# Performance work log

Measured on AMD Instinct MI355X. Metric: run time of the kernel, lower is better.

## Reference

```python
import jax, jax.numpy as jnp
import numpy as np

N, C_IN, C_K, C_V, H = 8192, 512, 512, 512, 8


def setup_inputs() -> dict:
    key = jax.random.key(0)
    ks = jax.random.split(key, 9)
    s = 0.02
    return {
        "input_": jax.random.normal(ks[0], (N, C_IN), dtype=jnp.float32),
        "Wk": jax.random.normal(ks[1], (C_IN, C_K), dtype=jnp.float32) * s,
        "bk": jnp.zeros((C_K,), dtype=jnp.float32),
        "Wq": jax.random.normal(ks[2], (C_IN, C_K), dtype=jnp.float32) * s,
        "bq": jnp.zeros((C_K,), dtype=jnp.float32),
        "Wv": jax.random.normal(ks[3], (C_IN, C_V), dtype=jnp.float32) * s,
        "bv": jnp.zeros((C_V,), dtype=jnp.float32),
        "Wr": jax.random.normal(ks[4], (C_K, C_K), dtype=jnp.float32) * s,
        "br": jnp.zeros((C_K,), dtype=jnp.float32),
    }


def reference(input_, Wk, bk, Wq, bq, Wv, bv, Wr, br):
    n = input_.shape[0]
    keys = input_ @ Wk + bk      # [N, C_K]
    queries = input_ @ Wq + bq   # [N, C_K]
    values = input_ @ Wv + bv    # [N, C_V]
    hk = C_K // H
    hv = C_V // H
    # [H, N, hk] / [H, N, hv]
    k = keys.reshape(n, H, hk).transpose(1, 0, 2)
    q = queries.reshape(n, H, hk).transpose(1, 0, 2)
    v = values.reshape(n, H, hv).transpose(1, 0, 2)
    k_sm = jax.nn.softmax(k, axis=1)   # softmax over tokens (dim=0 in torch)
    q_sm = jax.nn.softmax(q, axis=2)   # softmax over head channels (dim=1)
    # context = key^T @ value per head: [H, hk, hv]
    context = jnp.einsum('hnk,hnv->hkv', k_sm, v)
    attended = jnp.einsum('hnk,hkv->hnv', q_sm, context)  # [H, N, hv]
    # concat heads along channel dim -> [N, C_V]
    aggregated = attended.transpose(1, 0, 2).reshape(n, C_V)
    attention = aggregated @ Wr + br
    # mean over heads of q_sm @ k_sm^T; contracting h and k jointly = one GEMM
    scores = jnp.einsum('hnk,hmk->nm', q_sm, k_sm) / H  # [N, N]
    return attention, scores
```

## Files before the change

### kernel.cpp

```cpp
#include <hip/hip_runtime.h>

#define NT 8192
#define CD 512
#define NH 8
#define SC_N 8192

using f32x4  = __attribute__((ext_vector_type(4))) float;
using bf16x8 = __attribute__((ext_vector_type(8))) __bf16;

__device__ __forceinline__ unsigned short f2bf(float x) {
    union { float f; unsigned u; } c; c.f = x;
    unsigned r = c.u + 0x7fffu + ((c.u >> 16) & 1u);
    return (unsigned short)(r >> 16);
}
__device__ __forceinline__ float bf2f(unsigned short b) {
    union { float f; unsigned u; } c; c.u = ((unsigned)b) << 16;
    return c.f;
}

__global__ void prep_k(const float4* __restrict__ in, unsigned short* __restrict__ out,
                       const float* __restrict__ Wk, const float* __restrict__ Wq,
                       const float* __restrict__ Wv, const float* __restrict__ bk,
                       const float* __restrict__ bq, const float* __restrict__ bv,
                       unsigned short* __restrict__ Wt, float* __restrict__ biaskqv) {
    int b = blockIdx.x;
    if (b < 4096) {
        int i = b * 256 + threadIdx.x;
        float4 v = in[i];
        out[i*4+0] = f2bf(v.x);
        out[i*4+1] = f2bf(v.y);
        out[i*4+2] = f2bf(v.z);
        out[i*4+3] = f2bf(v.w);
    } else {
        int idx = (b - 4096) * 256 + threadIdx.x;
        int c = idx >> 9, k = idx & 511;
        int sec = c >> 9, cc = c & 511;
        const float* W = (sec == 0) ? Wk : ((sec == 1) ? Wq : Wv);
        Wt[idx] = f2bf(W[k * 512 + cc]);
        if (idx < 1536) {
            const float* bb = (idx < 512) ? bk : ((idx < 1024) ? bq : bv);
            biaskqv[idx] = bb[idx & 511];
        }
    }
}

__global__ __launch_bounds__(256) void kqv_gemm_k(
    const unsigned short* __restrict__ A, const unsigned short* __restrict__ Bt,
    const float* __restrict__ bias,
    unsigned short* __restrict__ kbf, unsigned short* __restrict__ qsm,
    unsigned short* __restrict__ vbf,
    float* __restrict__ pmax, float* __restrict__ psum)
{
    __shared__ unsigned short sA[128 * 32];
    __shared__ unsigned short sB[128 * 32];
    const int tid  = threadIdx.x;
    const int wid  = tid >> 6;
    const int lane = tid & 63;
    const int col0 = blockIdx.x * 128;
    const int row0 = blockIdx.y * 128;
    const int by   = blockIdx.y;
    const int wr = (wid >> 1) * 64;
    const int wc = (wid & 1) * 64;
    const int fr = lane & 15;
    const int fq = lane >> 4;
    const int srow = lane >> 2;
    const int scol = (lane & 3) * 8;

    f32x4 acc[4][4] = {};

    for (int kt = 0; kt < 16; ++kt) {
        const int k0 = kt << 5;
        __syncthreads();
        #pragma unroll
        for (int s = 0; s < 2; ++s) {
            const int seg = wid * 2 + s;
            const unsigned short* gA = A + (size_t)(row0 + seg * 16 + srow) * 512 + k0 + scol;
            __builtin_amdgcn_global_load_lds(
                (const __attribute__((address_space(1))) void*)gA,
                (__attribute__((address_space(3))) void*)(sA + seg * 512), 16, 0, 0);
            const unsigned short* gB = Bt + (size_t)(col0 + seg * 16 + srow) * 512 + k0 + scol;
            __builtin_amdgcn_global_load_lds(
                (const __attribute__((address_space(1))) void*)gB,
                (__attribute__((address_space(3))) void*)(sB + seg * 512), 16, 0, 0);
        }
        __syncthreads();

        bf16x8 av[4], bfrag[4];
        #pragma unroll
        for (int m = 0; m < 4; ++m)
            av[m] = *(const bf16x8*)(sA + (wr + m * 16 + fr) * 32 + fq * 8);
        #pragma unroll
        for (int n = 0; n < 4; ++n)
            bfrag[n] = *(const bf16x8*)(sB + (wc + n * 16 + fr) * 32 + fq * 8);
        #pragma unroll
        for (int m = 0; m < 4; ++m)
            #pragma unroll
            for (int n = 0; n < 4; ++n)
                acc[m][n] = __builtin_amdgcn_mfma_f32_16x16x32_bf16(av[m], bfrag[n], acc[m][n], 0, 0, 0);
    }

    const int sec = col0 >> 9;
    const int cs0 = (col0 & 511) + wc;

    if (sec == 0) {
        const int pb = by * 2 + (wr >> 6);
        #pragma unroll
        for (int n = 0; n < 4; ++n) {
            const int col = cs0 + n * 16 + fr;
            const float bv = bias[col];
            float vv[4][4], mx = -1e30f;
            #pragma unroll
            for (int m = 0; m < 4; ++m)
                #pragma unroll
                for (int r = 0; r < 4; ++r) {
                    float x = bf2f(f2bf(acc[m][n][r] + bv));
                    vv[m][r] = x; mx = fmaxf(mx, x);
                }
            mx = fmaxf(mx, __shfl_xor(mx, 16));
            mx = fmaxf(mx, __shfl_xor(mx, 32));
            float s = 0.f;
            #pragma unroll
            for (int m = 0; m < 4; ++m)
                #pragma unroll
                for (int r = 0; r < 4; ++r) {
                    s += __expf(vv[m][r] - mx);
                    kbf[(size_t)(row0 + wr + m * 16 + fq * 4 + r) * 512 + col] = f2bf(vv[m][r]);
                }
            s += __shfl_xor(s, 16);
            s += __shfl_xor(s, 32);
            if (lane < 16) { pmax[pb * 512 + col] = mx; psum[pb * 512 + col] = s; }
        }
    } else if (sec == 1) {
        #pragma unroll
        for (int m = 0; m < 4; ++m)
            #pragma unroll
            for (int r = 0; r < 4; ++r) {
                float e[4], mx = -1e30f;
                #pragma unroll
                for (int n = 0; n < 4; ++n) {
                    float x = bf2f(f2bf(acc[m][n][r] + bias[512 + cs0 + n * 16 + fr]));
                    e[n] = x; mx = fmaxf(mx, x);
                }
                mx = fmaxf(mx, __shfl_xor(mx, 1));
                mx = fmaxf(mx, __shfl_xor(mx, 2));
                mx = fmaxf(mx, __shfl_xor(mx, 4));
                mx = fmaxf(mx, __shfl_xor(mx, 8));
                float s = 0.f;
                #pragma unroll
                for (int n = 0; n < 4; ++n) { e[n] = __expf(e[n] - mx); s += e[n]; }
                s += __shfl_xor(s, 1);
                s += __shfl_xor(s, 2);
                s += __shfl_xor(s, 4);
                s += __shfl_xor(s, 8);
                const float rs = 1.f / s;
                const int row = row0 + wr + m * 16 + fq * 4 + r;
                #pragma unroll
                for (int n = 0; n < 4; ++n)
                    qsm[(size_t)row * 512 + cs0 + n * 16 + fr] = f2bf(e[n] * rs);
            }
    } else {
        #pragma unroll
        for (int n = 0; n < 4; ++n) {
            const int col = cs0 + n * 16 + fr;
            const float bv = bias[1024 + col];
            #pragma unroll
            for (int m = 0; m < 4; ++m)
                #pragma unroll
                for (int r = 0; r < 4; ++r)
                    vbf[(size_t)(row0 + wr + m * 16 + fq * 4 + r) * 512 + col] = f2bf(acc[m][n][r] + bv);
        }
    }
}

__global__ __launch_bounds__(256) void ksmctx_k(
    const unsigned short* __restrict__ kbf, const unsigned short* __restrict__ vbf,
    const float* __restrict__ pmax, const float* __restrict__ psum,
    unsigned short* __restrict__ ksm, float* __restrict__ pctx)
{
    const int ch = blockIdx.x;
    const int h  = blockIdx.y;
    const int tid = threadIdx.x, w = tid >> 6, lane = tid & 63;
    const int fr = lane & 15, fq = lane >> 4;
    __shared__ unsigned short tr[4][2][4096];
    __shared__ float redm[4][64], reds[4][64], cmx[64], crc[64];

    {
        const int c = tid & 63, q = tid >> 6;
        const int col = h * 64 + c;
        float m = -1e30f;
        for (int r = 0; r < 32; ++r) m = fmaxf(m, pmax[(q * 32 + r) * 512 + col]);
        float s = 0.f;
        for (int r = 0; r < 32; ++r)
            s += psum[(q * 32 + r) * 512 + col] * __expf(pmax[(q * 32 + r) * 512 + col] - m);
        redm[q][c] = m; reds[q][c] = s;
    }
    __syncthreads();
    if (tid < 64) {
        float m = fmaxf(fmaxf(redm[0][tid], redm[1][tid]), fmaxf(redm[2][tid], redm[3][tid]));
        float s = 0.f;
        #pragma unroll
        for (int q = 0; q < 4; ++q) s += reds[q][tid] * __expf(redm[q][tid] - m);
        cmx[tid] = m; crc[tid] = 1.f / s;
    }
    __syncthreads();

    char* kt = (char*)&tr[w][0][0];
    char* vt = (char*)&tr[w][1][0];
    const int nbase = ch * 256 + w * 64;
    #pragma unroll
    for (int j = 0; j < 8; ++j) {
        bf16x8 kv = *(const bf16x8*)(kbf + (size_t)(nbase + lane) * 512 + h * 64 + j * 8);
        bf16x8 vv = *(const bf16x8*)(vbf + (size_t)(nbase + lane) * 512 + h * 64 + j * 8);
        unsigned short ko[8];
        #pragma unroll
        for (int e = 0; e < 8; ++e) {
            int k = j * 8 + e;
            float x = __expf(bf2f(((const unsigned short*)&kv)[e]) - cmx[k]) * crc[k];
            unsigned short us = f2bf(x);
            ko[e] = us;
            int byte = (k * 128 + lane * 2) ^ (e << 4);
            *(unsigned short*)(kt + byte) = us;
            *(unsigned short*)(vt + byte) = ((const unsigned short*)&vv)[e];
        }
        *(uint4*)(ksm + (size_t)(nbase + lane) * 512 + h * 64 + j * 8) = *(const uint4*)ko;
    }
    asm volatile("s_waitcnt lgkmcnt(0)" ::: "memory");
    __builtin_amdgcn_sched_barrier(0);

    f32x4 acc[4][4] = {};
    #pragma unroll
    for (int ks = 0; ks < 2; ++ks) {
        bf16x8 a[4], b[4];
        #pragma unroll
        for (int mf = 0; mf < 4; ++mf) {
            int row  = mf * 16 + fr;
            int byte = (row * 128 + (ks * 4 + fq) * 16) ^ ((row & 7) << 4);
            a[mf] = *(const bf16x8*)(kt + byte);
            b[mf] = *(const bf16x8*)(vt + byte);
        }
        #pragma unroll
        for (int mf = 0; mf < 4; ++mf)
            #pragma unroll
            for (int nf = 0; nf < 4; ++nf)
                acc[mf][nf] = __builtin_amdgcn_mfma_f32_16x16x32_bf16(a[mf], b[nf], acc[mf][nf], 0, 0, 0);
    }

    float* red = (float*)&tr[w][0][0];
    #pragma unroll
    for (int mf = 0; mf < 4; ++mf)
        #pragma unroll
        for (int nf = 0; nf < 4; ++nf)
            #pragma unroll
            for (int r = 0; r < 4; ++r) {
                int lr = mf * 16 + fq * 4 + r;
                int lc = (nf * 16 + fr) ^ (((lr >> 2) & 1) << 4);
                red[lr * 64 + lc] = acc[mf][nf][r];
            }
    __syncthreads();
    const float* rbase = (const float*)&tr[0][0][0];
    float* out = pctx + (size_t)(ch * 8 + h) * 4096;
    #pragma unroll
    for (int it = 0; it < 16; ++it) {
        int e = it * 256 + tid;
        int lr = e >> 6;
        int ph = (lr * 64) + ((e & 63) ^ (((lr >> 2) & 1) << 4));
        float s = rbase[ph] + rbase[4096 + ph] + rbase[8192 + ph] + rbase[12288 + ph];
        out[e] = s;
    }
}

__global__ void mtred_k(const float* __restrict__ pctx, const float* __restrict__ Wr,
                        unsigned short* __restrict__ Mt) {
    __shared__ float cr[64];
    const int b = blockIdx.x;
    const int hk = b >> 1;
    const int o  = (b & 1) * 256 + threadIdx.x;
    const int h = hk >> 6, k = hk & 63;
    if (threadIdx.x < 64) {
        float s = 0.f;
        for (int p = 0; p < 32; ++p)
            s += pctx[(size_t)(p * 8 + h) * 4096 + k * 64 + threadIdx.x];
        cr[threadIdx.x] = s;
    }
    __syncthreads();
    const float* wp = Wr + (size_t)(h * 64) * 512 + o;
    float s = 0.f;
    #pragma unroll
    for (int j = 0; j < 64; ++j)
        s += cr[j] * wp[(size_t)j * 512];
    Mt[(size_t)o * 512 + hk] = f2bf(s);
}

__global__ __launch_bounds__(256) void scores_attn_k(
    const unsigned short* __restrict__ qsm, const unsigned short* __restrict__ ksm,
    const unsigned short* __restrict__ Mt, const float* __restrict__ br,
    float* __restrict__ attn_out, float* __restrict__ scores_out)
{
    __shared__ unsigned short sA[128 * 32];
    __shared__ unsigned short sB[128 * 32];
    const int tid  = threadIdx.x;
    const int wid  = tid >> 6;
    const int lane = tid & 63;
    const int wr = (wid >> 1) * 64;
    const int wc = (wid & 1) * 64;
    const int fr = lane & 15;
    const int fq = lane >> 4;
    const int srow = lane >> 2;
    const int scol = (lane & 3) * 8;

    const bool is_attn = blockIdx.x < 256;
    int row0, col0;
    const unsigned short* Bt;
    if (is_attn) {
        const int bx = blockIdx.x;
        col0 = (bx & 3) * 128;
        row0 = (bx >> 2) * 128;
        Bt = Mt;
    } else {
        int g = blockIdx.x - 256;
        g = (g & 7) * 512 + (g >> 3);
        row0 = ((g & 7) + ((g >> 9) << 3)) * 128;
        col0 = ((g >> 3) & 63) * 128;
        Bt = ksm;
    }

    f32x4 acc[4][4] = {};

    for (int kt = 0; kt < 16; ++kt) {
        const int k0 = kt << 5;
        __syncthreads();
        #pragma unroll
        for (int s = 0; s < 2; ++s) {
            const int seg = wid * 2 + s;
            const unsigned short* gA = qsm + (size_t)(row0 + seg * 16 + srow) * 512 + k0 + scol;
            __builtin_amdgcn_global_load_lds(
                (const __attribute__((address_space(1))) void*)gA,
                (__attribute__((address_space(3))) void*)(sA + seg * 512), 16, 0, 0);
            const unsigned short* gB = Bt + (size_t)(col0 + seg * 16 + srow) * 512 + k0 + scol;
            __builtin_amdgcn_global_load_lds(
                (const __attribute__((address_space(1))) void*)gB,
                (__attribute__((address_space(3))) void*)(sB + seg * 512), 16, 0, 0);
        }
        __syncthreads();

        bf16x8 av[4], bfrag[4];
        #pragma unroll
        for (int m = 0; m < 4; ++m)
            av[m] = *(const bf16x8*)(sA + (wr + m * 16 + fr) * 32 + fq * 8);
        #pragma unroll
        for (int n = 0; n < 4; ++n)
            bfrag[n] = *(const bf16x8*)(sB + (wc + n * 16 + fr) * 32 + fq * 8);
        #pragma unroll
        for (int m = 0; m < 4; ++m)
            #pragma unroll
            for (int n = 0; n < 4; ++n)
                acc[m][n] = __builtin_amdgcn_mfma_f32_16x16x32_bf16(av[m], bfrag[n], acc[m][n], 0, 0, 0);
    }

    if (is_attn) {
        #pragma unroll
        for (int n = 0; n < 4; ++n) {
            const int col = col0 + wc + n * 16 + fr;
            const float bval = br[col];
            #pragma unroll
            for (int m = 0; m < 4; ++m) {
                #pragma unroll
                for (int r = 0; r < 4; ++r) {
                    const int row = row0 + wr + m * 16 + fq * 4 + r;
                    __builtin_nontemporal_store(acc[m][n][r] + bval, &attn_out[(size_t)row * 512 + col]);
                }
            }
        }
    } else {
        #pragma unroll
        for (int n = 0; n < 4; ++n) {
            const int col = col0 + wc + n * 16 + fr;
            #pragma unroll
            for (int m = 0; m < 4; ++m) {
                #pragma unroll
                for (int r = 0; r < 4; ++r) {
                    const int row = row0 + wr + m * 16 + fq * 4 + r;
                    __builtin_nontemporal_store(acc[m][n][r] * 0.125f, &scores_out[(size_t)row * SC_N + col]);
                }
            }
        }
    }
}

extern "C" void kernel_launch(void* const* d_in, const int* in_sizes, int n_in,
                              void* d_out, int out_size, void* d_ws, size_t ws_size,
                              hipStream_t stream) {
    const float* input = (const float*)d_in[0];
    const float* Wk = (const float*)d_in[1];
    const float* bk = (const float*)d_in[2];
    const float* Wq = (const float*)d_in[3];
    const float* bq = (const float*)d_in[4];
    const float* Wv = (const float*)d_in[5];
    const float* bv = (const float*)d_in[6];
    const float* Wr = (const float*)d_in[7];
    const float* br = (const float*)d_in[8];

    char* ws = (char*)d_ws;
    unsigned short* inp_bf = (unsigned short*)ws;  ws += (size_t)NT * CD * 2;
    unsigned short* Wt     = (unsigned short*)ws;  ws += (size_t)1536 * 512 * 2;
    float* biaskqv         = (float*)ws;           ws += 1536 * 4;
    unsigned short* kbf    = (unsigned short*)ws;  ws += (size_t)NT * CD * 2;
    unsigned short* qsm    = (unsigned short*)ws;  ws += (size_t)NT * CD * 2;
    unsigned short* vbf    = (unsigned short*)ws;  ws += (size_t)NT * CD * 2;
    unsigned short* ksm    = (unsigned short*)ws;  ws += (size_t)NT * CD * 2;
    float* pmax            = (float*)ws;           ws += 128 * 512 * 4;
    float* psum            = (float*)ws;           ws += 128 * 512 * 4;
    float* pctx            = (float*)ws;           ws += (size_t)32 * 8 * 4096 * 4;
    unsigned short* Mt     = (unsigned short*)ws;  ws += (size_t)512 * 512 * 2;

    float* attn_out   = (float*)d_out;
    float* scores_out = (float*)d_out + (size_t)NT * CD;

    prep_k<<<7168, 256, 0, stream>>>((const float4*)input, inp_bf,
                                     Wk, Wq, Wv, bk, bq, bv, Wt, biaskqv);

    kqv_gemm_k<<<dim3(12, 64), 256, 0, stream>>>(inp_bf, Wt, biaskqv,
                                                 kbf, qsm, vbf, pmax, psum);

    ksmctx_k<<<dim3(32, 8), 256, 0, stream>>>(kbf, vbf, pmax, psum, ksm, pctx);

    mtred_k<<<1024, 256, 0, stream>>>(pctx, Wr, Mt);

    scores_attn_k<<<4352, 256, 0, stream>>>(qsm, ksm, Mt, br, attn_out, scores_out);
}
```

Baseline: 177.3 us.

## Double K-tile depth to 64 and XOR-swizzle LDS layout in scores GEMM

```diff
diff --git a/kernel.cpp b/kernel.cpp
--- a/kernel.cpp
+++ b/kernel.cpp
@@ -296,8 +296,8 @@
     const unsigned short* __restrict__ Mt, const float* __restrict__ br,
     float* __restrict__ attn_out, float* __restrict__ scores_out)
 {
-    __shared__ unsigned short sA[128 * 32];
-    __shared__ unsigned short sB[128 * 32];
+    __shared__ unsigned short sA[128 * 64];
+    __shared__ unsigned short sB[128 * 64];
     const int tid  = threadIdx.x;
     const int wid  = tid >> 6;
     const int lane = tid & 63;
@@ -305,8 +305,6 @@
     const int wc = (wid & 1) * 64;
     const int fr = lane & 15;
     const int fq = lane >> 4;
-    const int srow = lane >> 2;
-    const int scol = (lane & 3) * 8;
 
     const bool is_attn = blockIdx.x < 256;
     int row0, col0;
@@ -324,37 +322,58 @@
         Bt = ksm;
     }
 
+    int srow[4], sk8[4];
+    #pragma unroll
+    for (int l = 0; l < 4; ++l) {
+        int i = l * 256 + tid;
+        srow[l] = i >> 3;
+        sk8[l]  = ((i & 7) ^ ((i >> 3) & 7)) * 8;
+    }
+
+    int offA[4][2], offB[4][2];
+    #pragma unroll
+    for (int m = 0; m < 4; ++m)
+        #pragma unroll
+        for (int ks = 0; ks < 2; ++ks) {
+            int ra = wr + m * 16 + fr;
+            offA[m][ks] = ra * 128 + (((ks * 4 + fq) ^ (ra & 7)) << 4);
+            int rb = wc + m * 16 + fr;
+            offB[m][ks] = rb * 128 + (((ks * 4 + fq) ^ (rb & 7)) << 4);
+        }
+
     f32x4 acc[4][4] = {};
 
-    for (int kt = 0; kt < 16; ++kt) {
-        const int k0 = kt << 5;
+    for (int kt = 0; kt < 8; ++kt) {
+        const int k0 = kt << 6;
         __syncthreads();
         #pragma unroll
-        for (int s = 0; s < 2; ++s) {
-            const int seg = wid * 2 + s;
-            const unsigned short* gA = qsm + (size_t)(row0 + seg * 16 + srow) * 512 + k0 + scol;
+        for (int l = 0; l < 4; ++l) {
+            const unsigned short* gA = qsm + (size_t)(row0 + srow[l]) * 512 + k0 + sk8[l];
             __builtin_amdgcn_global_load_lds(
                 (const __attribute__((address_space(1))) void*)gA,
-                (__attribute__((address_space(3))) void*)(sA + seg * 512), 16, 0, 0);
-            const unsigned short* gB = Bt + (size_t)(col0 + seg * 16 + srow) * 512 + k0 + scol;
+                (__attribute__((address_space(3))) void*)(sA + (l * 256 + wid * 64) * 8), 16, 0, 0);
+            const unsigned short* gB = Bt + (size_t)(col0 + srow[l]) * 512 + k0 + sk8[l];
             __builtin_amdgcn_global_load_lds(
                 (const __attribute__((address_space(1))) void*)gB,
-                (__attribute__((address_space(3))) void*)(sB + seg * 512), 16, 0, 0);
+                (__attribute__((address_space(3))) void*)(sB + (l * 256 + wid * 64) * 8), 16, 0, 0);
         }
         __syncthreads();
 
-        bf16x8 av[4], bfrag[4];
+        bf16x8 av[4][2], bv[4][2];
         #pragma unroll
         for (int m = 0; m < 4; ++m)
-            av[m] = *(const bf16x8*)(sA + (wr + m * 16 + fr) * 32 + fq * 8);
-        #pragma unroll
-        for (int n = 0; n < 4; ++n)
-            bfrag[n] = *(const bf16x8*)(sB + (wc + n * 16 + fr) * 32 + fq * 8);
-        #pragma unroll
-        for (int m = 0; m < 4; ++m)
-            #pragma unroll
-            for (int n = 0; n < 4; ++n)
-                acc[m][n] = __builtin_amdgcn_mfma_f32_16x16x32_bf16(av[m], bfrag[n], acc[m][n], 0, 0, 0);
+            #pragma unroll
+            for (int ks = 0; ks < 2; ++ks) {
+                av[m][ks] = *(const bf16x8*)((const char*)sA + offA[m][ks]);
+                bv[m][ks] = *(const bf16x8*)((const char*)sB + offB[m][ks]);
+            }
+        #pragma unroll
+        for (int ks = 0; ks < 2; ++ks)
+            #pragma unroll
+            for (int m = 0; m < 4; ++m)
+                #pragma unroll
+                for (int n = 0; n < 4; ++n)
+                    acc[m][n] = __builtin_amdgcn_mfma_f32_16x16x32_bf16(av[m][ks], bv[n][ks], acc[m][n], 0, 0, 0);
     }
 
     if (is_attn) {
```

Result: slower. 183.8 us (+3.7%).

## Fuse Mt reduction into ksmctx via atomic counter and enlarge scores tile

Applied to the files above, without the earlier changes.

```diff
diff --git a/kernel.cpp b/kernel.cpp
--- a/kernel.cpp
+++ b/kernel.cpp
@@ -22,8 +22,10 @@
                        const float* __restrict__ Wk, const float* __restrict__ Wq,
                        const float* __restrict__ Wv, const float* __restrict__ bk,
                        const float* __restrict__ bq, const float* __restrict__ bv,
-                       unsigned short* __restrict__ Wt, float* __restrict__ biaskqv) {
+                       unsigned short* __restrict__ Wt, float* __restrict__ biaskqv,
+                       int* __restrict__ cnt) {
     int b = blockIdx.x;
+    if (b == 0 && threadIdx.x == 0) *cnt = 0;
     if (b < 4096) {
         int i = b * 256 + threadIdx.x;
         float4 v = in[i];
@@ -175,7 +177,9 @@
 __global__ __launch_bounds__(256) void ksmctx_k(
     const unsigned short* __restrict__ kbf, const unsigned short* __restrict__ vbf,
     const float* __restrict__ pmax, const float* __restrict__ psum,
-    unsigned short* __restrict__ ksm, float* __restrict__ pctx)
+    unsigned short* __restrict__ ksm, float* __restrict__ pctx,
+    const float* __restrict__ Wr, unsigned short* __restrict__ Mt,
+    int* __restrict__ cnt)
 {
     const int ch = blockIdx.x;
     const int h  = blockIdx.y;
@@ -183,6 +187,7 @@
     const int fr = lane & 15, fq = lane >> 4;
     __shared__ unsigned short tr[4][2][4096];
     __shared__ float redm[4][64], reds[4][64], cmx[64], crc[64];
+    __shared__ int lold;
 
     {
         const int c = tid & 63, q = tid >> 6;
@@ -267,28 +272,41 @@
         float s = rbase[ph] + rbase[4096 + ph] + rbase[8192 + ph] + rbase[12288 + ph];
         out[e] = s;
     }
-}
-
-__global__ void mtred_k(const float* __restrict__ pctx, const float* __restrict__ Wr,
-                        unsigned short* __restrict__ Mt) {
-    __shared__ float cr[64];
-    const int b = blockIdx.x;
-    const int hk = b >> 1;
-    const int o  = (b & 1) * 256 + threadIdx.x;
-    const int h = hk >> 6, k = hk & 63;
-    if (threadIdx.x < 64) {
-        float s = 0.f;
-        for (int p = 0; p < 32; ++p)
-            s += pctx[(size_t)(p * 8 + h) * 4096 + k * 64 + threadIdx.x];
-        cr[threadIdx.x] = s;
-    }
+
+    __threadfence();
     __syncthreads();
-    const float* wp = Wr + (size_t)(h * 64) * 512 + o;
-    float s = 0.f;
-    #pragma unroll
-    for (int j = 0; j < 64; ++j)
-        s += cr[j] * wp[(size_t)j * 512];
-    Mt[(size_t)o * 512 + hk] = f2bf(s);
+    if (tid == 0) lold = atomicAdd(cnt, 1);
+    __syncthreads();
+    const int old = lold;
+    if (old >= 224) {
+        if (tid == 0) { while (atomicAdd(cnt, 0) < 256) __builtin_amdgcn_s_sleep(2); }
+        __syncthreads();
+        __threadfence();
+        const int ti = old - 224;
+        float* cr = (float*)&tr[0][0][0];
+        for (int u = 0; u < 16; ++u) {
+            const int hk = ti * 16 + u;
+            const int hh = hk >> 6, kk = hk & 63;
+            if (tid < 64) {
+                float s = 0.f;
+                for (int p = 0; p < 32; ++p)
+                    s += pctx[(size_t)(p * 8 + hh) * 4096 + kk * 64 + tid];
+                cr[tid] = s;
+            }
+            __syncthreads();
+            const float* wp = Wr + (size_t)(hh * 64) * 512;
+            #pragma unroll
+            for (int half = 0; half < 2; ++half) {
+                const int o = half * 256 + tid;
+                float s = 0.f;
+                #pragma unroll
+                for (int j = 0; j < 64; ++j)
+                    s += cr[j] * wp[(size_t)j * 512 + o];
+                Mt[(size_t)o * 512 + hk] = f2bf(s);
+            }
+            __syncthreads();
+        }
+    }
 }
 
 __global__ __launch_bounds__(256) void scores_attn_k(
@@ -296,77 +314,78 @@
     const unsigned short* __restrict__ Mt, const float* __restrict__ br,
     float* __restrict__ attn_out, float* __restrict__ scores_out)
 {
-    __shared__ unsigned short sA[128 * 32];
+    __shared__ unsigned short sA[256 * 32];
     __shared__ unsigned short sB[128 * 32];
     const int tid  = threadIdx.x;
     const int wid  = tid >> 6;
     const int lane = tid & 63;
-    const int wr = (wid >> 1) * 64;
-    const int wc = (wid & 1) * 64;
+    const int wm = wid >> 1;
+    const int wn = wid & 1;
     const int fr = lane & 15;
     const int fq = lane >> 4;
-    const int srow = lane >> 2;
-    const int scol = (lane & 3) * 8;
-
-    const bool is_attn = blockIdx.x < 256;
+
+    const bool is_attn = blockIdx.x < 128;
     int row0, col0;
     const unsigned short* Bt;
     if (is_attn) {
-        const int bx = blockIdx.x;
-        col0 = (bx & 3) * 128;
-        row0 = (bx >> 2) * 128;
+        col0 = (blockIdx.x & 3) * 128;
+        row0 = (blockIdx.x >> 2) * 256;
         Bt = Mt;
     } else {
-        int g = blockIdx.x - 256;
-        g = (g & 7) * 512 + (g >> 3);
-        row0 = ((g & 7) + ((g >> 9) << 3)) * 128;
-        col0 = ((g >> 3) & 63) * 128;
+        int g = blockIdx.x - 128;
+        g = (g & 7) * 256 + (g >> 3);
+        row0 = (g >> 6) * 256;
+        col0 = (g & 63) * 128;
         Bt = ksm;
     }
 
-    f32x4 acc[4][4] = {};
+    f32x4 acc[8][4] = {};
 
     for (int kt = 0; kt < 16; ++kt) {
         const int k0 = kt << 5;
         __syncthreads();
         #pragma unroll
-        for (int s = 0; s < 2; ++s) {
-            const int seg = wid * 2 + s;
-            const unsigned short* gA = qsm + (size_t)(row0 + seg * 16 + srow) * 512 + k0 + scol;
+        for (int l = 0; l < 4; ++l) {
+            int i = l * 256 + tid;
+            const unsigned short* gA = qsm + (size_t)(row0 + (i >> 2)) * 512 + k0 + (i & 3) * 8;
             __builtin_amdgcn_global_load_lds(
                 (const __attribute__((address_space(1))) void*)gA,
-                (__attribute__((address_space(3))) void*)(sA + seg * 512), 16, 0, 0);
-            const unsigned short* gB = Bt + (size_t)(col0 + seg * 16 + srow) * 512 + k0 + scol;
+                (__attribute__((address_space(3))) void*)(sA + i * 8), 16, 0, 0);
+        }
+        #pragma unroll
+        for (int l = 0; l < 2; ++l) {
+            int i = l * 256 + tid;
+            const unsigned short* gB = Bt + (size_t)(col0 + (i >> 2)) * 512 + k0 + (i & 3) * 8;
             __builtin_amdgcn_global_load_lds(
                 (const __attribute__((address_space(1))) void*)gB,
-                (__attribute__((address_space(3))) void*)(sB + seg * 512), 16, 0, 0);
+                (__attribute__((address_space(3))) void*)(sB + i * 8), 16, 0, 0);
         }
         __syncthreads();
 
-        bf16x8 av[4], bfrag[4];
-        #pragma unroll
-        for (int m = 0; m < 4; ++m)
-            av[m] = *(const bf16x8*)(sA + (wr + m * 16 + fr) * 32 + fq * 8);
+        bf16x8 av[8], bv[4];
+        #pragma unroll
+        for (int m = 0; m < 8; ++m)
+            av[m] = *(const bf16x8*)(sA + (wm * 128 + m * 16 + fr) * 32 + fq * 8);
         #pragma unroll
         for (int n = 0; n < 4; ++n)
-            bfrag[n] = *(const bf16x8*)(sB + (wc + n * 16 + fr) * 32 + fq * 8);
-        #pragma unroll
-        for (int m = 0; m < 4; ++m)
-            #pragma unroll
-            for (int n = 0; n < 4; ++n)
-                acc[m][n] = __builtin_amdgcn_mfma_f32_16x16x32_bf16(av[m], bfrag[n], acc[m][n], 0, 0, 0);
+            bv[n] = *(const bf16x8*)(sB + (wn * 64 + n * 16 + fr) * 32 + fq * 8);
+        #pragma unroll
+        for (int n = 0; n < 4; ++n)
+            #pragma unroll
+            for (int m = 0; m < 8; ++m)
+                acc[m][n] = __builtin_amdgcn_mfma_f32_16x16x32_bf16(av[m], bv[n], acc[m][n], 0, 0, 0);
     }
 
     if (is_attn) {
         #pragma unroll
         for (int n = 0; n < 4; ++n) {
-            const int col = col0 + wc + n * 16 + fr;
+            const int col = col0 + wn * 64 + n * 16 + fr;
             const float bval = br[col];
             #pragma unroll
-            for (int m = 0; m < 4; ++m) {
+            for (int m = 0; m < 8; ++m) {
                 #pragma unroll
                 for (int r = 0; r < 4; ++r) {
-                    const int row = row0 + wr + m * 16 + fq * 4 + r;
+                    const int row = row0 + wm * 128 + m * 16 + fq * 4 + r;
                     __builtin_nontemporal_store(acc[m][n][r] + bval, &attn_out[(size_t)row * 512 + col]);
                 }
             }
@@ -374,12 +393,12 @@
     } else {
         #pragma unroll
         for (int n = 0; n < 4; ++n) {
-            const int col = col0 + wc + n * 16 + fr;
-            #pragma unroll
-            for (int m = 0; m < 4; ++m) {
+            const int col = col0 + wn * 64 + n * 16 + fr;
+            #pragma unroll
+            for (int m = 0; m < 8; ++m) {
                 #pragma unroll
                 for (int r = 0; r < 4; ++r) {
-                    const int row = row0 + wr + m * 16 + fq * 4 + r;
+                    const int row = row0 + wm * 128 + m * 16 + fq * 4 + r;
                     __builtin_nontemporal_store(acc[m][n][r] * 0.125f, &scores_out[(size_t)row * SC_N + col]);
                 }
             }
@@ -412,19 +431,19 @@
     float* psum            = (float*)ws;           ws += 128 * 512 * 4;
     float* pctx            = (float*)ws;           ws += (size_t)32 * 8 * 4096 * 4;
     unsigned short* Mt     = (unsigned short*)ws;  ws += (size_t)512 * 512 * 2;
+    int* cnt               = (int*)ws;             ws += 128;
 
     float* attn_out   = (float*)d_out;
     float* scores_out = (float*)d_out + (size_t)NT * CD;
 
     prep_k<<<7168, 256, 0, stream>>>((const float4*)input, inp_bf,
-                                     Wk, Wq, Wv, bk, bq, bv, Wt, biaskqv);
+                                     Wk, Wq, Wv, bk, bq, bv, Wt, biaskqv, cnt);
 
     kqv_gemm_k<<<dim3(12, 64), 256, 0, stream>>>(inp_bf, Wt, biaskqv,
                                                  kbf, qsm, vbf, pmax, psum);
 
-    ksmctx_k<<<dim3(32, 8), 256, 0, stream>>>(kbf, vbf, pmax, psum, ksm, pctx);
-
-    mtred_k<<<1024, 256, 0, stream>>>(pctx, Wr, Mt);
-
-    scores_attn_k<<<4352, 256, 0, stream>>>(qsm, ksm, Mt, br, attn_out, scores_out);
-}
+    ksmctx_k<<<dim3(32, 8), 256, 0, stream>>>(kbf, vbf, pmax, psum, ksm, pctx,
+                                              Wr, Mt, cnt);
+
+    scores_attn_k<<<2176, 256, 0, stream>>>(qsm, ksm, Mt, br, attn_out, scores_out);
+}
```

Measured after the change: 296.9 us. 1.67x slower.

## Double-buffer LDS tiles in scores_attn kernel to overlap loads with MFMA

Applied to the files above, without the earlier changes.

```diff
diff --git a/kernel.cpp b/kernel.cpp
--- a/kernel.cpp
+++ b/kernel.cpp
@@ -291,13 +291,13 @@
     Mt[(size_t)o * 512 + hk] = f2bf(s);
 }
 
-__global__ __launch_bounds__(256) void scores_attn_k(
+__global__ __launch_bounds__(256, 3) void scores_attn_k(
     const unsigned short* __restrict__ qsm, const unsigned short* __restrict__ ksm,
     const unsigned short* __restrict__ Mt, const float* __restrict__ br,
     float* __restrict__ attn_out, float* __restrict__ scores_out)
 {
-    __shared__ unsigned short sA[128 * 32];
-    __shared__ unsigned short sB[128 * 32];
+    __shared__ unsigned short sA0[128 * 32], sA1[128 * 32];
+    __shared__ unsigned short sB0[128 * 32], sB1[128 * 32];
     const int tid  = threadIdx.x;
     const int wid  = tid >> 6;
     const int lane = tid & 63;
@@ -326,35 +326,54 @@
 
     f32x4 acc[4][4] = {};
 
-    for (int kt = 0; kt < 16; ++kt) {
+    auto STAGE = [&](int kt, unsigned short* dA, unsigned short* dB) {
         const int k0 = kt << 5;
-        __syncthreads();
         #pragma unroll
         for (int s = 0; s < 2; ++s) {
             const int seg = wid * 2 + s;
             const unsigned short* gA = qsm + (size_t)(row0 + seg * 16 + srow) * 512 + k0 + scol;
             __builtin_amdgcn_global_load_lds(
                 (const __attribute__((address_space(1))) void*)gA,
-                (__attribute__((address_space(3))) void*)(sA + seg * 512), 16, 0, 0);
+                (__attribute__((address_space(3))) void*)(dA + seg * 512), 16, 0, 0);
             const unsigned short* gB = Bt + (size_t)(col0 + seg * 16 + srow) * 512 + k0 + scol;
             __builtin_amdgcn_global_load_lds(
                 (const __attribute__((address_space(1))) void*)gB,
-                (__attribute__((address_space(3))) void*)(sB + seg * 512), 16, 0, 0);
-        }
-        __syncthreads();
-
+                (__attribute__((address_space(3))) void*)(dB + seg * 512), 16, 0, 0);
+        }
+    };
+
+    auto BODY = [&](int kt, const unsigned short* cA, const unsigned short* cB,
+                    unsigned short* nA, unsigned short* nB) {
+        if (kt < 15) STAGE(kt + 1, nA, nB);
+        __builtin_amdgcn_sched_barrier(0);
         bf16x8 av[4], bfrag[4];
         #pragma unroll
         for (int m = 0; m < 4; ++m)
-            av[m] = *(const bf16x8*)(sA + (wr + m * 16 + fr) * 32 + fq * 8);
+            av[m] = *(const bf16x8*)(cA + (wr + m * 16 + fr) * 32 + fq * 8);
         #pragma unroll
         for (int n = 0; n < 4; ++n)
-            bfrag[n] = *(const bf16x8*)(sB + (wc + n * 16 + fr) * 32 + fq * 8);
+            bfrag[n] = *(const bf16x8*)(cB + (wc + n * 16 + fr) * 32 + fq * 8);
+        __builtin_amdgcn_s_setprio(1);
         #pragma unroll
         for (int m = 0; m < 4; ++m)
             #pragma unroll
             for (int n = 0; n < 4; ++n)
                 acc[m][n] = __builtin_amdgcn_mfma_f32_16x16x32_bf16(av[m], bfrag[n], acc[m][n], 0, 0, 0);
+        __builtin_amdgcn_s_setprio(0);
+        asm volatile("s_waitcnt vmcnt(0)" ::: "memory");
+        __builtin_amdgcn_s_barrier();
+        __builtin_amdgcn_sched_barrier(0);
+    };
+
+    STAGE(0, sA0, sB0);
+    asm volatile("s_waitcnt vmcnt(0)" ::: "memory");
+    __builtin_amdgcn_s_barrier();
+    __builtin_amdgcn_sched_barrier(0);
+
+    #pragma unroll
+    for (int kt = 0; kt < 16; kt += 2) {
+        BODY(kt,     sA0, sB0, sA1, sB1);
+        BODY(kt + 1, sA1, sB1, sA0, sB0);
     }
 
     if (is_attn) {
```

Measured after the change: 168.2 us, median of 2. 1.05x faster.
